# Performance work log

Measured on AMD Instinct MI355X. Metric: run time of the kernel, lower is better.

Reference implementation:

```python
import jax, jax.numpy as jnp
import numpy as np

N_NODES = 20000
D = 256            # input_dim (forced by 32x16 reshape: 2*D == 512)
N_EDGES = 320000


def _init(key, shape, scale=0.02):
    return scale * jax.random.normal(key, shape, jnp.float32)


def setup_inputs() -> dict:
    key = jax.random.key(0)
    ks = jax.random.split(key, 20)
    x = jax.random.normal(ks[0], (N_NODES, D), jnp.float32)
    edge = jax.random.randint(ks[1], (N_EDGES, 2), 0, N_NODES, dtype=jnp.int64)
    params = dict(
        W_gcn=_init(ks[2], (D, 2 * D)), b_gcn=jnp.zeros((2 * D,), jnp.float32),
        conv1_w=_init(ks[3], (1, 1, 3, 3)), conv1_b=jnp.zeros((1,), jnp.float32),
        conv2_w=_init(ks[4], (1, 1, 3, 3)), conv2_b=jnp.zeros((1,), jnp.float32),
        Wc1=_init(ks[5], (2 * D, 2 * D)), bc1=jnp.zeros((2 * D,), jnp.float32),
        Wc2=_init(ks[6], (2 * D, 2 * D)), bc2=jnp.zeros((2 * D,), jnp.float32),
        Wc3=_init(ks[7], (2 * D, 2 * D)), bc3=jnp.zeros((2 * D,), jnp.float32),
        Wp1=_init(ks[8], (4 * D, 2 * D)), bp1=jnp.zeros((2 * D,), jnp.float32),
        Wp2=_init(ks[9], (2 * D, D)), bp2=jnp.zeros((D,), jnp.float32),
        Wp3=_init(ks[10], (D, D // 2)), bp3=jnp.zeros((D // 2,), jnp.float32),
        Wp4=_init(ks[11], (D // 2, 2)), bp4=jnp.zeros((2,), jnp.float32),
    )
    return dict(x=x, edge=edge, **params)


def _gcn_conv(x, edge, W, b):
    # PyG GCNConv: add self-loops, symmetric deg^-1/2 normalization, scatter-add at dst
    src, dst = edge[:, 0], edge[:, 1]
    loops = jnp.arange(N_NODES, dtype=edge.dtype)
    src = jnp.concatenate([src, loops])
    dst = jnp.concatenate([dst, loops])
    xw = x @ W                                              # [N, 2D]
    deg = jax.ops.segment_sum(jnp.ones_like(dst, jnp.float32), dst, N_NODES)
    dinv = jnp.where(deg > 0, jax.lax.rsqrt(jnp.maximum(deg, 1e-12)), 0.0)
    norm = dinv[src] * dinv[dst]                            # [E+N]
    agg = jax.ops.segment_sum(norm[:, None] * xw[src], dst, N_NODES)
    return agg + b


def reference(x, edge, W_gcn, b_gcn, conv1_w, conv1_b, conv2_w, conv2_b,
              Wc1, bc1, Wc2, bc2, Wc3, bc3,
              Wp1, bp1, Wp2, bp2, Wp3, bp3, Wp4, bp4):
    # First stage: GCNConv + ReLU, then sum readout over nodes -> [1, 2D]
    h = jax.nn.relu(_gcn_conv(x, edge, W_gcn, b_gcn))
    h = jnp.sum(h, axis=0, keepdims=True)                   # [1, 512]

    img = h.reshape(1, 1, 32, 16)
    dn = ('NCHW', 'OIHW', 'NCHW')
    c = jax.nn.relu(jax.lax.conv_general_dilated(img, conv1_w, (1, 1), 'SAME', dimension_numbers=dn) + conv1_b.reshape(1, -1, 1, 1))
    c = jax.nn.relu(jax.lax.conv_general_dilated(c, conv2_w, (1, 1), 'SAME', dimension_numbers=dn) + conv2_b.reshape(1, -1, 1, 1))
    high_conf = jax.nn.softmax(c.reshape(1, -1), axis=1)    # [1, 512]

    # Second stage, branch B: 3-layer MLP with softmax
    f = jax.nn.relu(h @ Wc1 + bc1)
    f = jax.nn.relu(f @ Wc2 + bc2)
    front = jax.nn.softmax(f @ Wc3 + bc3, axis=1)           # [1, 512]

    complete = jnp.concatenate([high_conf, front], axis=1)  # [1, 1024]

    # Predictor MLP: 1024 -> 512 -> 256 -> 128 -> 2, sigmoid
    p = jax.nn.relu(complete @ Wp1 + bp1)
    p = jax.nn.relu(p @ Wp2 + bp2)
    p = jax.nn.relu(p @ Wp3 + bp3)
    pre = jax.nn.sigmoid(p @ Wp4 + bp4)                     # [1, 2]
    return pre
```

## Files before the change

### kernel.cpp

```cpp
#include <hip/hip_runtime.h>

#define N_NODES 20000
#define N_EDGES 320000
#define DD      256
#define D2      512
#define BCAP    64

typedef short short8 __attribute__((ext_vector_type(8)));
typedef float f32x4  __attribute__((ext_vector_type(4)));
typedef float f32x2  __attribute__((ext_vector_type(2)));

__device__ __forceinline__ unsigned f2b(float f) {
    unsigned u = __float_as_uint(f);
    u = u + 0x7fffu + ((u >> 16) & 1u);
    return u >> 16;
}

__device__ __forceinline__ unsigned f2e4m3(float f) {
    unsigned u = __float_as_uint(f);
    unsigned sg = (u >> 24) & 0x80u;
    float af = fabsf(f);
    if (af > 448.f) return sg | 0x7Eu;
    if (af < 0.015625f) {
        int i = (int)rintf(af * 512.f);
        return sg | (unsigned)i;
    }
    unsigned au = u & 0x7fffffffu;
    au += 0x7ffffu + ((au >> 20) & 1u);
    unsigned b = (au >> 20) - 960u;
    if (b > 0x7Eu) b = 0x7Eu;
    return sg | b;
}

__global__ void k1_prep(const int* __restrict__ edge, int* __restrict__ cnt,
                        int* __restrict__ csr, const float* __restrict__ x,
                        const float* __restrict__ Wg, unsigned short* __restrict__ WT,
                        unsigned* __restrict__ xf8) {
    int blk = blockIdx.x, tid = threadIdx.x;
    if (blk < 1250) {
        int e = blk * 256 + tid;
        if (e < N_EDGES) {
            int s = edge[2 * e], d = edge[2 * e + 1];
            int pos = atomicAdd(&cnt[d], 1);
            if (pos < BCAP) csr[d * BCAP + pos] = s;
        }
    } else if (blk < 1282) {
        int i = (blk - 1250) * 256 + tid;
        #pragma unroll
        for (int r = 0; r < 16; r++) {
            int idx = i + r * 8192;
            int k = idx >> 9, n = idx & 511;
            WT[n * 256 + k] = (unsigned short)f2b(Wg[idx]);
        }
    } else {
        int i = (blk - 1282) * 256 + tid;
        float4 v = ((const float4*)x)[i];
        xf8[i] = f2e4m3(v.x) | (f2e4m3(v.y) << 8) | (f2e4m3(v.z) << 16) | (f2e4m3(v.w) << 24);
    }
}

__device__ __forceinline__ float dinv_of(const int* cnt, int n) {
    return rsqrtf((float)(cnt[n] + 1));
}

__global__ void k4_agg(const int* __restrict__ cnt, const int* __restrict__ csr,
                       const unsigned char* __restrict__ xf8,
                       unsigned short* __restrict__ aggX) {
    int wid = threadIdx.x >> 6, lane = threadIdx.x & 63;
    int n = blockIdx.x * 4 + wid;
    float a0 = 0.f, a1 = 0.f, a2 = 0.f, a3 = 0.f;
    if (n < N_NODES) {
        int deg = cnt[n];
        if (deg > BCAP) deg = BCAP;
        const int* bkt = csr + n * BCAP;
        int e = 0;
        for (; e + 4 <= deg; e += 4) {
            int s0 = bkt[e], s1 = bkt[e + 1], s2 = bkt[e + 2], s3 = bkt[e + 3];
            unsigned u0 = *(const unsigned*)(xf8 + (size_t)s0 * DD + lane * 4);
            unsigned u1 = *(const unsigned*)(xf8 + (size_t)s1 * DD + lane * 4);
            unsigned u2 = *(const unsigned*)(xf8 + (size_t)s2 * DD + lane * 4);
            unsigned u3 = *(const unsigned*)(xf8 + (size_t)s3 * DD + lane * 4);
            float w0 = dinv_of(cnt, s0), w1 = dinv_of(cnt, s1);
            float w2 = dinv_of(cnt, s2), w3 = dinv_of(cnt, s3);
            f32x2 lo, hi;
            lo = __builtin_amdgcn_cvt_pk_f32_fp8(u0, false); hi = __builtin_amdgcn_cvt_pk_f32_fp8(u0, true);
            a0 += w0 * lo.x; a1 += w0 * lo.y; a2 += w0 * hi.x; a3 += w0 * hi.y;
            lo = __builtin_amdgcn_cvt_pk_f32_fp8(u1, false); hi = __builtin_amdgcn_cvt_pk_f32_fp8(u1, true);
            a0 += w1 * lo.x; a1 += w1 * lo.y; a2 += w1 * hi.x; a3 += w1 * hi.y;
            lo = __builtin_amdgcn_cvt_pk_f32_fp8(u2, false); hi = __builtin_amdgcn_cvt_pk_f32_fp8(u2, true);
            a0 += w2 * lo.x; a1 += w2 * lo.y; a2 += w2 * hi.x; a3 += w2 * hi.y;
            lo = __builtin_amdgcn_cvt_pk_f32_fp8(u3, false); hi = __builtin_amdgcn_cvt_pk_f32_fp8(u3, true);
            a0 += w3 * lo.x; a1 += w3 * lo.y; a2 += w3 * hi.x; a3 += w3 * hi.y;
        }
        for (; e < deg; e++) {
            int s = bkt[e];
            unsigned u = *(const unsigned*)(xf8 + (size_t)s * DD + lane * 4);
            float w = dinv_of(cnt, s);
            f32x2 lo = __builtin_amdgcn_cvt_pk_f32_fp8(u, false);
            f32x2 hi = __builtin_amdgcn_cvt_pk_f32_fp8(u, true);
            a0 += w * lo.x; a1 += w * lo.y; a2 += w * hi.x; a3 += w * hi.y;
        }
        float dn = dinv_of(cnt, n);
        unsigned u = *(const unsigned*)(xf8 + (size_t)n * DD + lane * 4);
        f32x2 lo = __builtin_amdgcn_cvt_pk_f32_fp8(u, false);
        f32x2 hi = __builtin_amdgcn_cvt_pk_f32_fp8(u, true);
        float dn2 = dn * dn;
        a0 = dn * a0 + dn2 * lo.x; a1 = dn * a1 + dn2 * lo.y;
        a2 = dn * a2 + dn2 * hi.x; a3 = dn * a3 + dn2 * hi.y;
    }
    uint2 o;
    o.x = f2b(a0) | (f2b(a1) << 16);
    o.y = f2b(a2) | (f2b(a3) << 16);
    *(uint2*)(aggX + (size_t)n * DD + lane * 4) = o;
}

#define TN 128
__global__ void __launch_bounds__(256, 2)
k5_gemm(const unsigned short* __restrict__ aggX, const unsigned short* __restrict__ WT,
        const float* __restrict__ bg, float* __restrict__ h) {
    __shared__ unsigned short bsh[TN * 264];
    __shared__ float hblk[TN];
    int tid = threadIdx.x;
    int rowblk = blockIdx.x;
    int ct = blockIdx.y;
    #pragma unroll
    for (int i = 0; i < 16; i++) {
        int c = tid + i * 256;
        int r = c >> 5;
        int kc = (c & 31) << 3;
        *(short8*)(&bsh[r * 264 + kc]) = *(const short8*)(WT + (size_t)(ct * TN + r) * DD + kc);
    }
    if (tid < TN) hblk[tid] = 0.f;
    __syncthreads();

    int w = tid >> 6, lane = tid & 63;
    int quad = lane >> 4, l15 = lane & 15;
    int row = rowblk * 64 + w * 16 + l15;
    f32x4 acc[8];
    #pragma unroll
    for (int nt = 0; nt < 8; nt++) acc[nt] = (f32x4){0.f, 0.f, 0.f, 0.f};
    #pragma unroll
    for (int kt = 0; kt < 8; kt++) {
        short8 a = *(const short8*)(aggX + (size_t)row * DD + kt * 32 + quad * 8);
        #pragma unroll
        for (int nt = 0; nt < 8; nt++) {
            short8 b = *(const short8*)(&bsh[(nt * 16 + l15) * 264 + kt * 32 + quad * 8]);
            acc[nt] = __builtin_amdgcn_mfma_f32_16x16x32_bf16(a, b, acc[nt], 0, 0, 0);
        }
    }
    int rowbase = rowblk * 64 + w * 16 + quad * 4;
    #pragma unroll
    for (int nt = 0; nt < 8; nt++) {
        int cl = nt * 16 + l15;
        float bias = bg[ct * TN + cl];
        float s = 0.f;
        #pragma unroll
        for (int r = 0; r < 4; r++) {
            if (rowbase + r < N_NODES) {
                float v = acc[nt][r] + bias;
                s += v > 0.f ? v : 0.f;
            }
        }
        atomicAdd(&hblk[cl], s);
    }
    __syncthreads();
    if (tid < TN) atomicAdd(&h[ct * TN + tid], hblk[tid]);
}

__global__ void k_mv(const float* __restrict__ in, const float* __restrict__ bias,
                     const float* __restrict__ W, float* __restrict__ out, int N, int act) {
    int c = blockIdx.y * 256 + threadIdx.x;
    int k0 = blockIdx.x * 8;
    float s = 0.f;
    #pragma unroll
    for (int kk = 0; kk < 8; kk++) {
        int k = k0 + kk;
        float v = in[k];
        if (act) { v += bias[k]; v = v > 0.f ? v : 0.f; }
        s += v * W[(size_t)k * N + c];
    }
    atomicAdd(&out[c], s);
}

__global__ void k9_mid(const float* __restrict__ h, const float* __restrict__ w1, const float* __restrict__ b1,
                       const float* __restrict__ w2, const float* __restrict__ b2,
                       const float* __restrict__ l3raw, const float* __restrict__ bc3,
                       float* __restrict__ complete) {
    __shared__ float img[512];
    __shared__ float c1s[512];
    __shared__ float red[512];
    int t = threadIdx.x;
    img[t] = h[t];
    __syncthreads();
    int y = t >> 4, x = t & 15;
    float s = 0.f;
    #pragma unroll
    for (int dy = -1; dy <= 1; dy++)
        #pragma unroll
        for (int dx = -1; dx <= 1; dx++) {
            int yy = y + dy, xc = x + dx;
            if (yy >= 0 && yy < 32 && xc >= 0 && xc < 16)
                s += w1[(dy + 1) * 3 + (dx + 1)] * img[yy * 16 + xc];
        }
    s += b1[0];
    c1s[t] = s > 0.f ? s : 0.f;
    __syncthreads();
    float s2 = 0.f;
    #pragma unroll
    for (int dy = -1; dy <= 1; dy++)
        #pragma unroll
        for (int dx = -1; dx <= 1; dx++) {
            int yy = y + dy, xc = x + dx;
            if (yy >= 0 && yy < 32 && xc >= 0 && xc < 16)
                s2 += w2[(dy + 1) * 3 + (dx + 1)] * c1s[yy * 16 + xc];
        }
    s2 += b2[0];
    float v2 = s2 > 0.f ? s2 : 0.f;
    red[t] = v2; __syncthreads();
    for (int off = 256; off > 0; off >>= 1) { if (t < off) red[t] = fmaxf(red[t], red[t + off]); __syncthreads(); }
    float m = red[0]; __syncthreads();
    float e = expf(v2 - m);
    red[t] = e; __syncthreads();
    for (int off = 256; off > 0; off >>= 1) { if (t < off) red[t] += red[t + off]; __syncthreads(); }
    complete[t] = e / red[0];
    __syncthreads();
    float z = l3raw[t] + bc3[t];
    red[t] = z; __syncthreads();
    for (int off = 256; off > 0; off >>= 1) { if (t < off) red[t] = fmaxf(red[t], red[t + off]); __syncthreads(); }
    float m2 = red[0]; __syncthreads();
    float e2 = expf(z - m2);
    red[t] = e2; __syncthreads();
    for (int off = 256; off > 0; off >>= 1) { if (t < off) red[t] += red[t + off]; __syncthreads(); }
    complete[512 + t] = e2 / red[0];
}

__global__ void k12_final(const float* __restrict__ p2raw, const float* __restrict__ bp2,
                          const float* __restrict__ Wp3, const float* __restrict__ bp3,
                          const float* __restrict__ Wp4, const float* __restrict__ bp4,
                          float* __restrict__ out) {
    __shared__ float p2s[256];
    __shared__ float p3s[128];
    int t = threadIdx.x;
    float v = p2raw[t] + bp2[t];
    p2s[t] = v > 0.f ? v : 0.f;
    __syncthreads();
    if (t < 128) {
        float s = bp3[t];
        #pragma unroll 8
        for (int k = 0; k < 256; k++) s += p2s[k] * Wp3[k * 128 + t];
        p3s[t] = s > 0.f ? s : 0.f;
    }
    __syncthreads();
    if (t < 2) {
        float s = bp4[t];
        for (int k = 0; k < 128; k++) s += p3s[k] * Wp4[k * 2 + t];
        out[t] = 1.f / (1.f + expf(-s));
    }
}

extern "C" void kernel_launch(void* const* d_in, const int* in_sizes, int n_in,
                              void* d_out, int out_size, void* d_ws, size_t ws_size,
                              hipStream_t stream) {
    const float* x    = (const float*)d_in[0];
    const int*   edge = (const int*)d_in[1];
    const float* Wg   = (const float*)d_in[2];
    const float* bg   = (const float*)d_in[3];
    const float* c1w  = (const float*)d_in[4];
    const float* c1b  = (const float*)d_in[5];
    const float* c2w  = (const float*)d_in[6];
    const float* c2b  = (const float*)d_in[7];
    const float* Wc1  = (const float*)d_in[8];
    const float* bc1  = (const float*)d_in[9];
    const float* Wc2  = (const float*)d_in[10];
    const float* bc2  = (const float*)d_in[11];
    const float* Wc3  = (const float*)d_in[12];
    const float* bc3  = (const float*)d_in[13];
    const float* Wp1  = (const float*)d_in[14];
    const float* bp1  = (const float*)d_in[15];
    const float* Wp2  = (const float*)d_in[16];
    const float* bp2  = (const float*)d_in[17];
    const float* Wp3  = (const float*)d_in[18];
    const float* bp3  = (const float*)d_in[19];
    const float* Wp4  = (const float*)d_in[20];
    const float* bp4  = (const float*)d_in[21];
    float* out = (float*)d_out;

    char* ws = (char*)d_ws;
    int*   cnt      = (int*)(ws + 0);
    float* h        = (float*)(ws + 80000);
    float* f1raw    = (float*)(ws + 82048);
    float* f2raw    = (float*)(ws + 84096);
    float* l3raw    = (float*)(ws + 86144);
    float* p1raw    = (float*)(ws + 88192);
    float* p2raw    = (float*)(ws + 90240);
    float* complete = (float*)(ws + 91264);
    int*   csr      = (int*)(ws + 95360);
    unsigned short* WT   = (unsigned short*)(ws + 5215360);
    unsigned short* aggX = (unsigned short*)(ws + 5477504);
    unsigned char*  xf8  = (unsigned char*)(ws + 15733888);
    (void)ws_size; (void)in_sizes; (void)n_in; (void)out_size;

    hipMemsetAsync(d_ws, 0, 91264, stream);

    k1_prep<<<6282, 256, 0, stream>>>(edge, cnt, csr, x, Wg, WT, (unsigned*)xf8);
    k4_agg<<<5008, 256, 0, stream>>>(cnt, csr, xf8, aggX);
    k5_gemm<<<dim3(313, 4), 256, 0, stream>>>(aggX, WT, bg, h);
    k_mv<<<dim3(64, 2), 256, 0, stream>>>(h,     nullptr, Wc1, f1raw, 512, 0);
    k_mv<<<dim3(64, 2), 256, 0, stream>>>(f1raw, bc1,     Wc2, f2raw, 512, 1);
    k_mv<<<dim3(64, 2), 256, 0, stream>>>(f2raw, bc2,     Wc3, l3raw, 512, 1);
    k9_mid<<<1, 512, 0, stream>>>(h, c1w, c1b, c2w, c2b, l3raw, bc3, complete);
    k_mv<<<dim3(128, 2), 256, 0, stream>>>(complete, nullptr, Wp1, p1raw, 512, 0);
    k_mv<<<dim3(64, 1), 256, 0, stream>>>(p1raw, bp1, Wp2, p2raw, 256, 1);
    k12_final<<<1, 256, 0, stream>>>(p2raw, bp2, Wp3, bp3, Wp4, bp4, out);
}
```

Baseline: 217.0 us.

## Fuse GCN aggregation and GEMM into one kernel via shared-memory tile

Merges the neighbor-aggregation kernel and the bf16 MFMA GEMM into a single kernel. Each block aggregates 32 node rows into LDS as bf16, then streams W in 64-column chunks through LDS and reduces relu(xW+b) into the per-block column sums. This removes the global round trip of the aggregated matrix and one launch. In exchange it uses only 626 blocks, each of which reloads all of W, and it serializes the gather phase before the matmul.

```diff
diff --git a/kernel.cpp b/kernel.cpp
--- a/kernel.cpp
+++ b/kernel.cpp
@@ -59,112 +59,111 @@
     }
 }
 
+#define ROWS 32
 __device__ __forceinline__ float dinv_of(const int* cnt, int n) {
     return rsqrtf((float)(cnt[n] + 1));
 }
 
-__global__ void k4_agg(const int* __restrict__ cnt, const int* __restrict__ csr,
-                       const unsigned char* __restrict__ xf8,
-                       unsigned short* __restrict__ aggX) {
-    int wid = threadIdx.x >> 6, lane = threadIdx.x & 63;
-    int n = blockIdx.x * 4 + wid;
-    float a0 = 0.f, a1 = 0.f, a2 = 0.f, a3 = 0.f;
-    if (n < N_NODES) {
-        int deg = cnt[n];
-        if (deg > BCAP) deg = BCAP;
-        const int* bkt = csr + n * BCAP;
-        int e = 0;
-        for (; e + 4 <= deg; e += 4) {
-            int s0 = bkt[e], s1 = bkt[e + 1], s2 = bkt[e + 2], s3 = bkt[e + 3];
-            unsigned u0 = *(const unsigned*)(xf8 + (size_t)s0 * DD + lane * 4);
-            unsigned u1 = *(const unsigned*)(xf8 + (size_t)s1 * DD + lane * 4);
-            unsigned u2 = *(const unsigned*)(xf8 + (size_t)s2 * DD + lane * 4);
-            unsigned u3 = *(const unsigned*)(xf8 + (size_t)s3 * DD + lane * 4);
-            float w0 = dinv_of(cnt, s0), w1 = dinv_of(cnt, s1);
-            float w2 = dinv_of(cnt, s2), w3 = dinv_of(cnt, s3);
-            f32x2 lo, hi;
-            lo = __builtin_amdgcn_cvt_pk_f32_fp8(u0, false); hi = __builtin_amdgcn_cvt_pk_f32_fp8(u0, true);
-            a0 += w0 * lo.x; a1 += w0 * lo.y; a2 += w0 * hi.x; a3 += w0 * hi.y;
-            lo = __builtin_amdgcn_cvt_pk_f32_fp8(u1, false); hi = __builtin_amdgcn_cvt_pk_f32_fp8(u1, true);
-            a0 += w1 * lo.x; a1 += w1 * lo.y; a2 += w1 * hi.x; a3 += w1 * hi.y;
-            lo = __builtin_amdgcn_cvt_pk_f32_fp8(u2, false); hi = __builtin_amdgcn_cvt_pk_f32_fp8(u2, true);
-            a0 += w2 * lo.x; a1 += w2 * lo.y; a2 += w2 * hi.x; a3 += w2 * hi.y;
-            lo = __builtin_amdgcn_cvt_pk_f32_fp8(u3, false); hi = __builtin_amdgcn_cvt_pk_f32_fp8(u3, true);
-            a0 += w3 * lo.x; a1 += w3 * lo.y; a2 += w3 * hi.x; a3 += w3 * hi.y;
-        }
-        for (; e < deg; e++) {
-            int s = bkt[e];
-            unsigned u = *(const unsigned*)(xf8 + (size_t)s * DD + lane * 4);
-            float w = dinv_of(cnt, s);
+__global__ void __launch_bounds__(256, 3)
+k45_fused(const int* __restrict__ cnt, const int* __restrict__ csr,
+          const unsigned char* __restrict__ xf8, const unsigned short* __restrict__ WT,
+          const float* __restrict__ bg, float* __restrict__ h) {
+    __shared__ unsigned short ash[ROWS * 264];
+    __shared__ unsigned short bsh[64 * 264];
+    __shared__ float hblk[D2];
+    int tid = threadIdx.x;
+    int w = tid >> 6, lane = tid & 63;
+    int rowblk = blockIdx.x;
+
+    for (int i = 0; i < 8; i++) {
+        int rloc = w * 8 + i;
+        int n = rowblk * ROWS + rloc;
+        float a0 = 0.f, a1 = 0.f, a2 = 0.f, a3 = 0.f;
+        if (n < N_NODES) {
+            int deg = cnt[n];
+            if (deg > BCAP) deg = BCAP;
+            const int* bkt = csr + n * BCAP;
+            int e = 0;
+            for (; e + 4 <= deg; e += 4) {
+                int s0 = bkt[e], s1 = bkt[e + 1], s2 = bkt[e + 2], s3 = bkt[e + 3];
+                unsigned u0 = *(const unsigned*)(xf8 + (size_t)s0 * DD + lane * 4);
+                unsigned u1 = *(const unsigned*)(xf8 + (size_t)s1 * DD + lane * 4);
+                unsigned u2 = *(const unsigned*)(xf8 + (size_t)s2 * DD + lane * 4);
+                unsigned u3 = *(const unsigned*)(xf8 + (size_t)s3 * DD + lane * 4);
+                float w0 = dinv_of(cnt, s0), w1 = dinv_of(cnt, s1);
+                float w2 = dinv_of(cnt, s2), w3 = dinv_of(cnt, s3);
+                f32x2 lo, hi;
+                lo = __builtin_amdgcn_cvt_pk_f32_fp8(u0, false); hi = __builtin_amdgcn_cvt_pk_f32_fp8(u0, true);
+                a0 += w0 * lo.x; a1 += w0 * lo.y; a2 += w0 * hi.x; a3 += w0 * hi.y;
+                lo = __builtin_amdgcn_cvt_pk_f32_fp8(u1, false); hi = __builtin_amdgcn_cvt_pk_f32_fp8(u1, true);
+                a0 += w1 * lo.x; a1 += w1 * lo.y; a2 += w1 * hi.x; a3 += w1 * hi.y;
+                lo = __builtin_amdgcn_cvt_pk_f32_fp8(u2, false); hi = __builtin_amdgcn_cvt_pk_f32_fp8(u2, true);
+                a0 += w2 * lo.x; a1 += w2 * lo.y; a2 += w2 * hi.x; a3 += w2 * hi.y;
+                lo = __builtin_amdgcn_cvt_pk_f32_fp8(u3, false); hi = __builtin_amdgcn_cvt_pk_f32_fp8(u3, true);
+                a0 += w3 * lo.x; a1 += w3 * lo.y; a2 += w3 * hi.x; a3 += w3 * hi.y;
+            }
+            for (; e < deg; e++) {
+                int s = bkt[e];
+                unsigned u = *(const unsigned*)(xf8 + (size_t)s * DD + lane * 4);
+                float wv = dinv_of(cnt, s);
+                f32x2 lo = __builtin_amdgcn_cvt_pk_f32_fp8(u, false);
+                f32x2 hi = __builtin_amdgcn_cvt_pk_f32_fp8(u, true);
+                a0 += wv * lo.x; a1 += wv * lo.y; a2 += wv * hi.x; a3 += wv * hi.y;
+            }
+            float dn = dinv_of(cnt, n);
+            unsigned u = *(const unsigned*)(xf8 + (size_t)n * DD + lane * 4);
             f32x2 lo = __builtin_amdgcn_cvt_pk_f32_fp8(u, false);
             f32x2 hi = __builtin_amdgcn_cvt_pk_f32_fp8(u, true);
-            a0 += w * lo.x; a1 += w * lo.y; a2 += w * hi.x; a3 += w * hi.y;
-        }
-        float dn = dinv_of(cnt, n);
-        unsigned u = *(const unsigned*)(xf8 + (size_t)n * DD + lane * 4);
-        f32x2 lo = __builtin_amdgcn_cvt_pk_f32_fp8(u, false);
-        f32x2 hi = __builtin_amdgcn_cvt_pk_f32_fp8(u, true);
-        float dn2 = dn * dn;
-        a0 = dn * a0 + dn2 * lo.x; a1 = dn * a1 + dn2 * lo.y;
-        a2 = dn * a2 + dn2 * hi.x; a3 = dn * a3 + dn2 * hi.y;
-    }
-    uint2 o;
-    o.x = f2b(a0) | (f2b(a1) << 16);
-    o.y = f2b(a2) | (f2b(a3) << 16);
-    *(uint2*)(aggX + (size_t)n * DD + lane * 4) = o;
-}
-
-#define TN 128
-__global__ void __launch_bounds__(256, 2)
-k5_gemm(const unsigned short* __restrict__ aggX, const unsigned short* __restrict__ WT,
-        const float* __restrict__ bg, float* __restrict__ h) {
-    __shared__ unsigned short bsh[TN * 264];
-    __shared__ float hblk[TN];
-    int tid = threadIdx.x;
-    int rowblk = blockIdx.x;
-    int ct = blockIdx.y;
-    #pragma unroll
-    for (int i = 0; i < 16; i++) {
-        int c = tid + i * 256;
-        int r = c >> 5;
-        int kc = (c & 31) << 3;
-        *(short8*)(&bsh[r * 264 + kc]) = *(const short8*)(WT + (size_t)(ct * TN + r) * DD + kc);
-    }
-    if (tid < TN) hblk[tid] = 0.f;
-    __syncthreads();
-
-    int w = tid >> 6, lane = tid & 63;
+            float dn2 = dn * dn;
+            a0 = dn * a0 + dn2 * lo.x; a1 = dn * a1 + dn2 * lo.y;
+            a2 = dn * a2 + dn2 * hi.x; a3 = dn * a3 + dn2 * hi.y;
+        }
+        uint2 o;
+        o.x = f2b(a0) | (f2b(a1) << 16);
+        o.y = f2b(a2) | (f2b(a3) << 16);
+        *(uint2*)(&ash[rloc * 264 + lane * 4]) = o;
+    }
+    hblk[tid] = 0.f; hblk[tid + 256] = 0.f;
+    __syncthreads();
+
     int quad = lane >> 4, l15 = lane & 15;
-    int row = rowblk * 64 + w * 16 + l15;
-    f32x4 acc[8];
-    #pragma unroll
-    for (int nt = 0; nt < 8; nt++) acc[nt] = (f32x4){0.f, 0.f, 0.f, 0.f};
-    #pragma unroll
-    for (int kt = 0; kt < 8; kt++) {
-        short8 a = *(const short8*)(aggX + (size_t)row * DD + kt * 32 + quad * 8);
-        #pragma unroll
-        for (int nt = 0; nt < 8; nt++) {
-            short8 b = *(const short8*)(&bsh[(nt * 16 + l15) * 264 + kt * 32 + quad * 8]);
-            acc[nt] = __builtin_amdgcn_mfma_f32_16x16x32_bf16(a, b, acc[nt], 0, 0, 0);
-        }
-    }
-    int rowbase = rowblk * 64 + w * 16 + quad * 4;
-    #pragma unroll
-    for (int nt = 0; nt < 8; nt++) {
-        int cl = nt * 16 + l15;
-        float bias = bg[ct * TN + cl];
-        float s = 0.f;
-        #pragma unroll
-        for (int r = 0; r < 4; r++) {
-            if (rowbase + r < N_NODES) {
-                float v = acc[nt][r] + bias;
-                s += v > 0.f ? v : 0.f;
+    int strip = w >> 1;
+    int cpair = w & 1;
+    int rowbase = rowblk * ROWS + strip * 16 + quad * 4;
+    for (int ch = 0; ch < 8; ch++) {
+        #pragma unroll
+        for (int i = 0; i < 8; i++) {
+            int u = tid + i * 256;
+            int r = u >> 5, kp = (u & 31) << 3;
+            *(short8*)(&bsh[r * 264 + kp]) = *(const short8*)(WT + (size_t)(ch * 64 + r) * DD + kp);
+        }
+        __syncthreads();
+        #pragma unroll
+        for (int t2 = 0; t2 < 2; t2++) {
+            int ctile = cpair * 2 + t2;
+            f32x4 acc = (f32x4){0.f, 0.f, 0.f, 0.f};
+            #pragma unroll
+            for (int kt = 0; kt < 8; kt++) {
+                short8 a = *(const short8*)(&ash[(strip * 16 + l15) * 264 + kt * 32 + quad * 8]);
+                short8 b = *(const short8*)(&bsh[(ctile * 16 + l15) * 264 + kt * 32 + quad * 8]);
+                acc = __builtin_amdgcn_mfma_f32_16x16x32_bf16(a, b, acc, 0, 0, 0);
             }
-        }
-        atomicAdd(&hblk[cl], s);
-    }
-    __syncthreads();
-    if (tid < TN) atomicAdd(&h[ct * TN + tid], hblk[tid]);
+            int col = ch * 64 + ctile * 16 + l15;
+            float bias = bg[col];
+            float s = 0.f;
+            #pragma unroll
+            for (int r = 0; r < 4; r++) {
+                if (rowbase + r < N_NODES) {
+                    float v = acc[r] + bias;
+                    s += v > 0.f ? v : 0.f;
+                }
+            }
+            atomicAdd(&hblk[col], s);
+        }
+        __syncthreads();
+    }
+    atomicAdd(&h[tid], hblk[tid]);
+    atomicAdd(&h[tid + 256], hblk[tid + 256]);
 }
 
 __global__ void k_mv(const float* __restrict__ in, const float* __restrict__ bias,
@@ -296,15 +295,13 @@
     float* complete = (float*)(ws + 91264);
     int*   csr      = (int*)(ws + 95360);
     unsigned short* WT   = (unsigned short*)(ws + 5215360);
-    unsigned short* aggX = (unsigned short*)(ws + 5477504);
-    unsigned char*  xf8  = (unsigned char*)(ws + 15733888);
+    unsigned char*  xf8  = (unsigned char*)(ws + 5477504);
     (void)ws_size; (void)in_sizes; (void)n_in; (void)out_size;
 
     hipMemsetAsync(d_ws, 0, 91264, stream);
 
     k1_prep<<<6282, 256, 0, stream>>>(edge, cnt, csr, x, Wg, WT, (unsigned*)xf8);
-    k4_agg<<<5008, 256, 0, stream>>>(cnt, csr, xf8, aggX);
-    k5_gemm<<<dim3(313, 4), 256, 0, stream>>>(aggX, WT, bg, h);
+    k45_fused<<<626, 256, 0, stream>>>(cnt, csr, xf8, WT, bg, h);
     k_mv<<<dim3(64, 2), 256, 0, stream>>>(h,     nullptr, Wc1, f1raw, 512, 0);
     k_mv<<<dim3(64, 2), 256, 0, stream>>>(f1raw, bc1,     Wc2, f2raw, 512, 1);
     k_mv<<<dim3(64, 2), 256, 0, stream>>>(f2raw, bc2,     Wc3, l3raw, 512, 1);
```

New measurement: 233.1 us. 7.4% more time.
